# Performance work log

Hardware: AMD Instinct MI355X
Metric: run time of the kernel (lower is better)

## Reference

```python
import jax, jax.numpy as jnp
import numpy as np

WIN, DIL, PAD, H = 5, 1, 2, 8  # window, dilation, unfold padding, num_heads
C = 256
EPS = 1e-5

def _ln(z, g, b):
    m = jnp.mean(z, axis=-1, keepdims=True)
    v = jnp.mean((z - m) ** 2, axis=-1, keepdims=True)
    return (z - m) * jax.lax.rsqrt(v + EPS) * g + b

def setup_inputs() -> dict:
    key = jax.random.key(0)
    ks = jax.random.split(key, 16)
    s = 0.02
    d = {
        'x': jax.random.normal(ks[0], (32, C, 64, 25), jnp.float32),
        'ln1_g': jnp.ones((C,), jnp.float32), 'ln1_b': jnp.zeros((C,), jnp.float32),
        'q_w': jax.random.normal(ks[1], (C, C)) * s, 'q_b': jnp.zeros((C,)),
        'qa_w': jax.random.normal(ks[2], (C, H)) * s, 'qa_b': jnp.zeros((H,)),
        'k_w': jax.random.normal(ks[3], (C, C)) * s, 'k_b': jnp.zeros((C,)),
        'ka_w': jax.random.normal(ks[4], (C, H)) * s, 'ka_b': jnp.zeros((H,)),
        'v_w': jax.random.normal(ks[5], (C, C)) * s, 'v_b': jnp.zeros((C,)),
        't_w': jax.random.normal(ks[6], (C, C)) * s, 't_b': jnp.zeros((C,)),
        'p_w': jax.random.normal(ks[7], (C, C)) * s, 'p_b': jnp.zeros((C,)),
        'ffn_g': jnp.ones((C,)), 'ffn_b': jnp.zeros((C,)),
        'w1': jax.random.normal(ks[8], (C, C)) * s, 'b1': jnp.zeros((C,)),
        'w2': jax.random.normal(ks[9], (C, C)) * s, 'b2': jnp.zeros((C,)),
    }
    return d

def reference(x, ln1_g, ln1_b, q_w, q_b, qa_w, qa_b, k_w, k_b, ka_w, ka_b,
              v_w, v_b, t_w, t_b, p_w, p_b, ffn_g, ffn_b, w1, b1, w2, b2):
    N, Cc, T, V = x.shape
    hc = Cc // H
    scale = 1.0 / np.sqrt(hc)
    B, L = N * T, WIN * V
    xp = jnp.pad(x, ((0, 0), (0, 0), (PAD, PAD), (0, 0)))
    win = jnp.stack([xp[:, :, k * DIL:k * DIL + T, :] for k in range(WIN)], axis=2)  # (N,C,W,T,V)
    wx = win.transpose(0, 3, 2, 4, 1).reshape(B, L, Cc)
    nx = _ln(wx, ln1_g, ln1_b)
    # attention: softmax-pooled query
    q = nx @ q_w + q_b                                      # (B,L,C)
    qw = jax.nn.softmax(((q @ qa_w + qa_b) * scale).transpose(0, 2, 1), axis=-1)  # (B,H,L)
    qh = q.reshape(B, L, H, hc).transpose(0, 2, 1, 3)       # (B,H,L,hc)
    pq = jnp.einsum('bhl,bhld->bhd', qw, qh)                # (B,H,hc)
    k_ = nx @ k_w + k_b
    kq = k_ * pq.reshape(B, 1, Cc)
    kw = jax.nn.softmax(((kq @ ka_w + ka_b) * scale).transpose(0, 2, 1), axis=-1)
    kh = k_.reshape(B, L, H, hc).transpose(0, 2, 1, 3)
    pk = jnp.einsum('bhl,bhld->bhd', kw, kh)                # (B,H,hc)
    v_ = nx @ v_w + v_b
    vh = v_.reshape(B, L, H, hc).transpose(0, 2, 1, 3)
    kv = (vh * pk[:, :, None, :]).transpose(0, 2, 1, 3).reshape(B, L, Cc)
    kvh = (kv @ t_w + t_b).reshape(B, L, H, hc).transpose(0, 2, 1, 3)
    att = ((kvh + qh).transpose(0, 2, 1, 3).reshape(B, L, Cc)) @ p_w + p_b
    # average over window, residual with flattened x
    att = att.reshape(B, WIN, V, Cc).mean(axis=1)           # (B,V,C)
    att = att + x.transpose(0, 2, 3, 1).reshape(B, V, Cc)
    # FFN residual block
    f = _ln(att, ffn_g, ffn_b)
    f = jax.nn.gelu(f @ w1 + b1, approximate=False) @ w2 + b2
    y = f + att
    return y.reshape(N, T, V, Cc).transpose(0, 3, 1, 2)     # (N,C,T,V)
```

## Files before the change

### kernel.cpp

```cpp
#include <hip/hip_runtime.h>
#include <hip/hip_bf16.h>

typedef unsigned short u16b;
typedef __attribute__((ext_vector_type(8))) short short8;
typedef __attribute__((ext_vector_type(4))) float floatx4;

#define DEV static __device__ __forceinline__

DEV float sh2f(unsigned short s) { union { unsigned u; float f; } c; c.u = ((unsigned)s) << 16; return c.f; }
DEV unsigned short f2b(float f) {
    unsigned u = __float_as_uint(f);
    u += 0x7FFF + ((u >> 16) & 1);
    return (unsigned short)(u >> 16);
}

constexpr int O_LN1G = 0, O_LN1B = 256, O_QB = 512, O_KB = 768, O_VB = 1024,
              O_TB = 1280, O_PB = 1536, O_FFNG = 1792, O_FFNB = 2048,
              O_B1 = 2304, O_B2 = 2560, O_QAB = 2816, O_KAB = 2824,
              O_QAW = 2832, O_KAW = 4880, O_CV = 6928;

__global__ void detect_k(const unsigned* __restrict__ xw, int* __restrict__ flag) {
    __shared__ int cnt;
    if (threadIdx.x == 0) cnt = 0;
    __syncthreads();
    int my = 0;
    for (int i = threadIdx.x; i < 4096; i += 256) {
        unsigned w = xw[i];
        unsigned e0 = (w >> 7) & 0xFFu;
        if (e0 >= 0xC0u) my++;
    }
    atomicAdd(&cnt, my);
    __syncthreads();
    if (threadIdx.x == 0) flag[0] = (cnt > 64) ? 1 : 0;
}

DEV unsigned short load_cvt(const void* src, size_t idx, int fp32) {
    return fp32 ? f2b(((const float*)src)[idx]) : ((const u16b*)src)[idx];
}

struct VecTab { const void* p[15]; int off[15]; int n[15]; };

__global__ __launch_bounds__(256)
void convert_vecs_k(VecTab tab, const int* __restrict__ flag, u16b* __restrict__ sv) {
    int e = blockIdx.x, fp32 = flag[0];
    const void* s = tab.p[e];
    int n = tab.n[e], off = tab.off[e];
    for (int i = threadIdx.x; i < n; i += 256)
        sv[off + i] = load_cvt(s, i, fp32);
}

struct W8 { const void* p[8]; unsigned dstoff[8]; unsigned rstride[8]; };

__global__ void wtrans_k(W8 tab, u16b* __restrict__ base, const int* __restrict__ flag) {
    __shared__ u16b tile[32][33];
    int fp32 = flag[0];
    const void* src = tab.p[blockIdx.z];
    u16b* dst = base + tab.dstoff[blockIdx.z];
    unsigned rs = tab.rstride[blockIdx.z];
    int c0 = blockIdx.x * 32, r0 = blockIdx.y * 32;
    int tx = threadIdx.x, ty = threadIdx.y;
#pragma unroll
    for (int i = 0; i < 32; i += 8)
        tile[ty + i][tx] = load_cvt(src, (size_t)(r0 + ty + i) * 256 + c0 + tx, fp32);
    __syncthreads();
#pragma unroll
    for (int i = 0; i < 32; i += 8)
        dst[(size_t)(c0 + ty + i) * rs + r0 + tx] = tile[tx][ty + i];
}

__global__ void transpose_in_k(const void* __restrict__ src, u16b* __restrict__ dst,
                               int rows, int cols, const int* __restrict__ flag) {
    __shared__ u16b tile[32][33];
    int fp32 = flag[0];
    int c0 = blockIdx.x * 32, r0 = blockIdx.y * 32;
    size_t zb = (size_t)blockIdx.z * rows * cols;
    int tx = threadIdx.x, ty = threadIdx.y;
#pragma unroll
    for (int i = 0; i < 32; i += 8)
        tile[ty + i][tx] = load_cvt(src, zb + (size_t)(r0 + ty + i) * cols + c0 + tx, fp32);
    __syncthreads();
#pragma unroll
    for (int i = 0; i < 32; i += 8)
        dst[zb + (size_t)(c0 + ty + i) * rows + r0 + tx] = tile[tx][ty + i];
}

__global__ void transpose_out_k(const u16b* __restrict__ src, void* __restrict__ dst,
                                int rows, int cols, const int* __restrict__ flag) {
    __shared__ u16b tile[32][33];
    int fp32 = flag[0];
    int c0 = blockIdx.x * 32, r0 = blockIdx.y * 32;
    size_t zb = (size_t)blockIdx.z * rows * cols;
    int tx = threadIdx.x, ty = threadIdx.y;
#pragma unroll
    for (int i = 0; i < 32; i += 8)
        tile[ty + i][tx] = src[zb + (size_t)(r0 + ty + i) * cols + c0 + tx];
    __syncthreads();
#pragma unroll
    for (int i = 0; i < 32; i += 8) {
        size_t idx = zb + (size_t)(c0 + ty + i) * rows + r0 + tx;
        unsigned short v = tile[tx][ty + i];
        if (fp32) ((float*)dst)[idx] = sh2f(v);
        else      ((u16b*)dst)[idx] = v;
    }
}

__global__ __launch_bounds__(256)
void rowstats_k(const u16b* __restrict__ src, float2* __restrict__ st,
                int valid, int total) {
    int wv = threadIdx.x >> 6, lane = threadIdx.x & 63;
    int r = blockIdx.x * 4 + wv;
    if (r >= total) return;
    if (r >= valid) { if (lane == 0) st[r] = make_float2(0.f, 0.f); return; }
    int c = lane * 4;
    ushort4 raw = *(const ushort4*)&src[(size_t)r * 256 + c];
    float x0 = sh2f(raw.x), x1 = sh2f(raw.y), x2 = sh2f(raw.z), x3 = sh2f(raw.w);
    float s  = x0 + x1 + x2 + x3;
    float sq = x0 * x0 + x1 * x1 + x2 * x2 + x3 * x3;
#pragma unroll
    for (int o = 32; o; o >>= 1) { s += __shfl_xor(s, o); sq += __shfl_xor(sq, o); }
    float mean = s * (1.f / 256.f);
    float var  = sq * (1.f / 256.f) - mean * mean;
    if (lane == 0) st[r] = make_float2(mean, rsqrtf(var + 1e-5f));
}

__global__ __launch_bounds__(256)
void cvec_k(const u16b* __restrict__ pT, u16b* __restrict__ sv) {
    int j = threadIdx.x;
    float acc = sh2f(sv[O_PB + j]);
    const u16b* row = pT + (size_t)j * 256;
    for (int i = 0; i < 256; i += 8) {
        short8 t8 = *(const short8*)&sv[O_TB + i];
        short8 p8 = *(const short8*)&row[i];
#pragma unroll
        for (int u = 0; u < 8; ++u)
            acc += sh2f((unsigned short)t8[u]) * sh2f((unsigned short)p8[u]);
    }
    sv[O_CV + j] = f2b(acc);
}

template <int EPI, int LNA>
__global__ __launch_bounds__(256)
void gemm256(const u16b* __restrict__ A, int aStride, int K,
             const u16b* __restrict__ Wt,
             const u16b* __restrict__ bias, const u16b* __restrict__ addm,
             u16b* __restrict__ out, size_t osParam,
             const float2* __restrict__ stats,
             const u16b* __restrict__ gvec, const u16b* __restrict__ bvec) {
    __shared__ u16b As[128 * 72];
    __shared__ u16b Bs[128 * 72];
    __shared__ float sg[256], sb[256];
    const int tid = threadIdx.x;
    const int m0 = blockIdx.x * 128, n0 = blockIdx.y * 128;
    const int wv = tid >> 6, lane = tid & 63;
    const int wrow = (wv >> 1) * 64, wcol = (wv & 1) * 64;
    const int fr = lane & 15;
    const int fq = lane >> 4;
    floatx4 acc[4][4];
    const floatx4 zero = {0.f, 0.f, 0.f, 0.f};
#pragma unroll
    for (int i = 0; i < 4; ++i)
#pragma unroll
        for (int j = 0; j < 4; ++j) acc[i][j] = zero;

    float2 strow[4];
    if (LNA) {
        sg[tid] = sh2f(gvec[tid]);
        sb[tid] = sh2f(bvec[tid]);
#pragma unroll
        for (int kk = 0; kk < 4; ++kk) strow[kk] = stats[m0 + (tid >> 3) + kk * 32];
        __syncthreads();
    }

    for (int kt = 0; kt < K; kt += 64) {
#pragma unroll
        for (int kk = 0; kk < 4; ++kk) {
            int chunk = tid + kk * 256;
            int row = chunk >> 3, col = (chunk & 7) * 8;
            union { uint4 u; unsigned short h[8]; } rw;
            rw.u = *(const uint4*)&A[(size_t)(m0 + row) * aStride + kt + col];
            if (LNA) {
#pragma unroll
                for (int j = 0; j < 8; ++j) {
                    float f = sh2f(rw.h[j]);
                    f = (f - strow[kk].x) * strow[kk].y * sg[kt + col + j] + sb[kt + col + j];
                    rw.h[j] = f2b(f);
                }
            }
            *(uint4*)&As[row * 72 + col] = rw.u;
            *(uint4*)&Bs[row * 72 + col] = *(const uint4*)&Wt[(size_t)(n0 + row) * K + kt + col];
        }
        __syncthreads();
#pragma unroll
        for (int s = 0; s < 2; ++s) {
            short8 af[4], bfr[4];
#pragma unroll
            for (int i = 0; i < 4; ++i)
                af[i] = *(short8*)&As[(wrow + i * 16 + fr) * 72 + s * 32 + fq * 8];
#pragma unroll
            for (int j = 0; j < 4; ++j)
                bfr[j] = *(short8*)&Bs[(wcol + j * 16 + fr) * 72 + s * 32 + fq * 8];
#pragma unroll
            for (int i = 0; i < 4; ++i)
#pragma unroll
                for (int j = 0; j < 4; ++j)
                    acc[i][j] = __builtin_amdgcn_mfma_f32_16x16x32_bf16(af[i], bfr[j], acc[i][j], 0, 0, 0);
        }
        __syncthreads();
    }
    float bv[4];
#pragma unroll
    for (int j = 0; j < 4; ++j) bv[j] = bias ? sh2f(bias[n0 + wcol + j * 16 + fr]) : 0.f;
#pragma unroll
    for (int i = 0; i < 4; ++i) {
#pragma unroll
        for (int r = 0; r < 4; ++r) {
            int row = m0 + wrow + i * 16 + fq * 4 + r;
            size_t ro = (size_t)row * 256;
#pragma unroll
            for (int j = 0; j < 4; ++j) {
                int col = n0 + wcol + j * 16 + fr;
                float val = acc[i][j][r] + bv[j];
                if (EPI == 2) val += sh2f(addm[ro + col]);
                if (EPI == 3) val = 0.5f * val * (1.0f + erff(val * 0.70710678118654752f));
                if (EPI == 4)      out[(size_t)(col >> 8) * osParam + ro + (col & 255)] = f2b(val);
                else if (EPI == 0) out[(size_t)row * osParam + col] = f2b(val);
                else               out[ro + col] = f2b(val);
            }
        }
    }
}

DEV void pool_stage(const u16b* __restrict__ S, const u16b* __restrict__ sv,
                    int awoff, int aboff, const float* mult, float* outPool,
                    const int* srow, u16b* su, float* slog, float* spool, int tid) {
    for (int i = tid; i < 2048; i += 512) {
        int c = i >> 3, h = i & 7;
        float w = sh2f(sv[awoff + i]);
        if (mult) w *= mult[c];
        su[h * 260 + c] = f2b(w);
    }
    __syncthreads();
    int wv = tid >> 6, lane = tid & 63;
    int fr = lane & 15, fq = lane >> 4;
    floatx4 acc = {0.f, 0.f, 0.f, 0.f};
    const u16b* Ar = S + (size_t)srow[wv * 16 + fr] * 256;
#pragma unroll
    for (int s = 0; s < 8; ++s) {
        short8 a  = *(const short8*)&Ar[s * 32 + fq * 8];
        short8 bb = *(const short8*)&su[fr * 260 + s * 32 + fq * 8];
        acc = __builtin_amdgcn_mfma_f32_16x16x32_bf16(a, bb, acc, 0, 0, 0);
    }
    float abv = sh2f(sv[aboff + (fr & 7)]);
    if (fr < 8) {
#pragma unroll
        for (int r = 0; r < 4; ++r)
            slog[(wv * 16 + fq * 4 + r) * 9 + fr] = (acc[r] + abv) * 0.17677669529663687f;
    }
    __syncthreads();
    {
        int h = wv;
        float v0 = (lane < 125) ? slog[lane * 9 + h] : -1e30f;
        float v1 = (lane + 64 < 125) ? slog[(lane + 64) * 9 + h] : -1e30f;
        float mx = fmaxf(v0, v1);
#pragma unroll
        for (int o = 32; o; o >>= 1) mx = fmaxf(mx, __shfl_xor(mx, o));
        float e0 = (lane < 125) ? __expf(v0 - mx) : 0.f;
        float e1 = (lane + 64 < 125) ? __expf(v1 - mx) : 0.f;
        float s = e0 + e1;
#pragma unroll
        for (int o = 32; o; o >>= 1) s += __shfl_xor(s, o);
        float inv = 1.f / s;
        if (lane < 125) slog[lane * 9 + h] = e0 * inv;
        if (lane + 64 < 125) slog[(lane + 64) * 9 + h] = e1 * inv;
    }
    __syncthreads();
    int c8 = (tid & 31) * 8, ls = tid >> 5;
    int h2 = c8 >> 5;
    float a8[8] = {0.f, 0.f, 0.f, 0.f, 0.f, 0.f, 0.f, 0.f};
    for (int l = ls; l < 125; l += 16) {
        float w = slog[l * 9 + h2];
        short8 d8 = *(const short8*)&S[(size_t)srow[l] * 256 + c8];
#pragma unroll
        for (int j = 0; j < 8; ++j) a8[j] += w * sh2f((unsigned short)d8[j]);
    }
#pragma unroll
    for (int j = 0; j < 8; ++j) spool[ls * 260 + c8 + j] = a8[j];
    __syncthreads();
    if (tid < 256) {
        float s = 0.f;
#pragma unroll
        for (int q = 0; q < 16; ++q) s += spool[q * 260 + tid];
        outPool[tid] = s;
    }
    __syncthreads();
}

__global__ __launch_bounds__(512)
void pool_fused(const u16b* __restrict__ qf, const u16b* __restrict__ kf,
                const u16b* __restrict__ vf, const u16b* __restrict__ sv,
                u16b* __restrict__ CB) {
    __shared__ int srow[128];
    __shared__ u16b su[16 * 260];
    __shared__ float slog[128 * 9];
    __shared__ float spool[16 * 260];
    __shared__ float spq[256], spk[256];
    int bid = blockIdx.x;
    int b = ((bid & 7) << 8) | (bid >> 3);
    int n = b >> 6, t = b & 63;
    int tid = threadIdx.x;
    if (tid < 128) {
        int l = tid < 125 ? tid : 124;
        int w = l / 25, v = l - w * 25, tt = t + w - 2;
        srow[tid] = ((unsigned)tt < 64u) ? (n * 64 + tt) * 25 + v : 51200;
    }
    for (int i = tid; i < 8 * 260; i += 512) su[8 * 260 + i] = 0;
    __syncthreads();
    pool_stage(qf, sv, O_QAW, O_QAB, nullptr, spq, srow, su, slog, spool, tid);
    for (int i = tid; i < 800; i += 512) {
        int v = i >> 5, c8 = (i & 31) * 8;
        float s[8] = {0.f, 0.f, 0.f, 0.f, 0.f, 0.f, 0.f, 0.f};
#pragma unroll
        for (int w = 0; w < 5; ++w) {
            short8 d8 = *(const short8*)&qf[(size_t)srow[w * 25 + v] * 256 + c8];
#pragma unroll
            for (int j = 0; j < 8; ++j) s[j] += sh2f((unsigned short)d8[j]);
        }
        unsigned short o[8];
#pragma unroll
        for (int j = 0; j < 8; ++j) o[j] = f2b(s[j] * 0.2f);
        *(uint4*)&CB[((size_t)b * 25 + v) * 512 + 256 + c8] = *(uint4*)o;
    }
    pool_stage(kf, sv, O_KAW, O_KAB, spq, spk, srow, su, slog, spool, tid);
    for (int i = tid; i < 800; i += 512) {
        int v = i >> 5, c8 = (i & 31) * 8;
        float s[8] = {0.f, 0.f, 0.f, 0.f, 0.f, 0.f, 0.f, 0.f};
#pragma unroll
        for (int w = 0; w < 5; ++w) {
            short8 d8 = *(const short8*)&vf[(size_t)srow[w * 25 + v] * 256 + c8];
#pragma unroll
            for (int j = 0; j < 8; ++j) s[j] += sh2f((unsigned short)d8[j]);
        }
        unsigned short o[8];
#pragma unroll
        for (int j = 0; j < 8; ++j) o[j] = f2b(s[j] * 0.2f * spk[c8 + j]);
        *(uint4*)&CB[((size_t)b * 25 + v) * 512 + c8] = *(uint4*)o;
    }
}

extern "C" void kernel_launch(void* const* d_in, const int* in_sizes, int n_in,
                              void* d_out, int out_size, void* d_ws, size_t ws_size,
                              hipStream_t stream) {
    (void)in_sizes; (void)n_in; (void)out_size; (void)ws_size;
    const void* x    = d_in[0];
    const void* ln1g = d_in[1];  const void* ln1b = d_in[2];
    const void* q_w  = d_in[3];  const void* q_b  = d_in[4];
    const void* qa_w = d_in[5];  const void* qa_b = d_in[6];
    const void* k_w  = d_in[7];  const void* k_b  = d_in[8];
    const void* ka_w = d_in[9];  const void* ka_b = d_in[10];
    const void* v_w  = d_in[11]; const void* v_b  = d_in[12];
    const void* t_w  = d_in[13]; const void* t_b  = d_in[14];
    const void* p_w  = d_in[15]; const void* p_b  = d_in[16];
    const void* ffng = d_in[17]; const void* ffnb = d_in[18];
    const void* w1   = d_in[19]; const void* b1   = d_in[20];
    const void* w2   = d_in[21]; const void* b2   = d_in[22];

    char* ws = (char*)d_ws;
    size_t off = 0;
    auto alloc = [&](size_t bytes) { void* p = ws + off; off += (bytes + 255) & ~(size_t)255; return p; };
    const size_t RPAD = 51328;
    int*    flag = (int*)alloc(256);
    u16b*   sv   = (u16b*)alloc(8192 * 2);
    u16b*   wT   = (u16b*)alloc((size_t)7 * 65536 * 2);
    u16b*   cW   = (u16b*)alloc((size_t)256 * 512 * 2);
    u16b*   xT   = (u16b*)alloc(RPAD * 256 * 2);
    u16b*   Bq   = (u16b*)alloc(RPAD * 256 * 2);
    u16b*   Bk   = (u16b*)alloc(RPAD * 256 * 2);
    u16b*   Bv   = (u16b*)alloc(RPAD * 256 * 2);
    u16b*   CB   = (u16b*)alloc((size_t)51200 * 512 * 2);
    u16b*   att  = (u16b*)alloc((size_t)51200 * 256 * 2);
    float2* st1  = (float2*)alloc(RPAD * 8);
    float2* st2  = (float2*)alloc((size_t)51200 * 8);

    u16b* pT  = wT + 3 * 65536;
    u16b* tT  = wT + 4 * 65536;
    u16b* w1T = wT + 5 * 65536;
    u16b* w2T = wT + 6 * 65536;

    detect_k<<<1, 256, 0, stream>>>((const unsigned*)x, flag);
    VecTab tab;
    const void* vp[15] = {ln1g, ln1b, q_b, k_b, v_b, t_b, p_b, ffng, ffnb, b1, b2, qa_b, ka_b, qa_w, ka_w};
    const int vo[15] = {O_LN1G, O_LN1B, O_QB, O_KB, O_VB, O_TB, O_PB, O_FFNG, O_FFNB, O_B1, O_B2, O_QAB, O_KAB, O_QAW, O_KAW};
    const int vn[15] = {256, 256, 256, 256, 256, 256, 256, 256, 256, 256, 256, 8, 8, 2048, 2048};
    for (int i = 0; i < 15; ++i) { tab.p[i] = vp[i]; tab.off[i] = vo[i]; tab.n[i] = vn[i]; }
    convert_vecs_k<<<15, 256, 0, stream>>>(tab, flag, sv);

    dim3 tb(32, 8);
    W8 wt;
    const void* wsrc[8] = {q_w, k_w, v_w, p_w, t_w, w1, w2, p_w};
    for (int i = 0; i < 8; ++i) {
        wt.p[i] = wsrc[i];
        wt.dstoff[i] = (i < 7) ? (unsigned)(i * 65536) : (unsigned)((cW + 256) - wT);
        wt.rstride[i] = (i < 7) ? 256u : 512u;
    }
    wtrans_k<<<dim3(8, 8, 8), tb, 0, stream>>>(wt, wT, flag);
    cvec_k<<<1, 256, 0, stream>>>(pT, sv);
    gemm256<0, 0><<<dim3(2, 2), 256, 0, stream>>>(pT, 256, 256, tT, nullptr, nullptr,
                                                  cW, 512, nullptr, nullptr, nullptr);
    transpose_in_k<<<dim3(50, 8, 32), tb, 0, stream>>>(x, xT, 256, 1600, flag);
    rowstats_k<<<12832, 256, 0, stream>>>(xT, st1, 51200, 51328);
    gemm256<4, 1><<<dim3(401, 6), 256, 0, stream>>>(xT, 256, 256, wT, sv + O_QB, nullptr,
                                                    Bq, RPAD * 256, st1, sv + O_LN1G, sv + O_LN1B);
    pool_fused<<<2048, 512, 0, stream>>>(Bq, Bk, Bv, sv, CB);
    gemm256<2, 0><<<dim3(400, 2), 256, 0, stream>>>(CB, 512, 512, cW, sv + O_CV, xT,
                                                    att, 256, nullptr, nullptr, nullptr);
    rowstats_k<<<12800, 256, 0, stream>>>(att, st2, 51200, 51200);
    gemm256<3, 1><<<dim3(400, 2), 256, 0, stream>>>(att, 256, 256, w1T, sv + O_B1, nullptr,
                                                    Bq, 256, st2, sv + O_FFNG, sv + O_FFNB);
    gemm256<2, 0><<<dim3(400, 2), 256, 0, stream>>>(Bq, 256, 256, w2T, sv + O_B2, att,
                                                    att, 256, nullptr, nullptr, nullptr);
    transpose_out_k<<<dim3(8, 50, 32), tb, 0, stream>>>(att, d_out, 1600, 256, flag);
}
```

Before: 420.9 us.

## Vectorize transposes and fuse query pooling with window-mean pass in pool kernel

The input and output transpose kernels now use 1D 256-thread blocks in which each thread moves four elements with float4/ushort4 loads and stores, and the shared tile is padded to 36 columns. This replaces scalar per-element global accesses. In pool_fused, the softmax-weighted query pooling is merged into the loop that computes the window mean of q, so each q row is read once instead of twice. The separate zeroing of part of the shared buffer is dropped. The 36-column padding may cause more bank conflicts on the column-wise shared reads, and zero-padded MFMA rows in logits_stage now depend on leftover shared contents.

```diff
diff --git a/kernel.cpp b/kernel.cpp
--- a/kernel.cpp
+++ b/kernel.cpp
@@ -68,39 +68,54 @@
         dst[(size_t)(c0 + ty + i) * rs + r0 + tx] = tile[tx][ty + i];
 }
 
-__global__ void transpose_in_k(const void* __restrict__ src, u16b* __restrict__ dst,
-                               int rows, int cols, const int* __restrict__ flag) {
-    __shared__ u16b tile[32][33];
+__global__ __launch_bounds__(256)
+void transpose_in_k(const void* __restrict__ src, u16b* __restrict__ dst,
+                    int rows, int cols, const int* __restrict__ flag) {
+    __shared__ u16b tile[32][36];
     int fp32 = flag[0];
     int c0 = blockIdx.x * 32, r0 = blockIdx.y * 32;
     size_t zb = (size_t)blockIdx.z * rows * cols;
-    int tx = threadIdx.x, ty = threadIdx.y;
-#pragma unroll
-    for (int i = 0; i < 32; i += 8)
-        tile[ty + i][tx] = load_cvt(src, zb + (size_t)(r0 + ty + i) * cols + c0 + tx, fp32);
-    __syncthreads();
-#pragma unroll
-    for (int i = 0; i < 32; i += 8)
-        dst[zb + (size_t)(c0 + ty + i) * rows + r0 + tx] = tile[tx][ty + i];
-}
-
-__global__ void transpose_out_k(const u16b* __restrict__ src, void* __restrict__ dst,
-                                int rows, int cols, const int* __restrict__ flag) {
-    __shared__ u16b tile[32][33];
+    int tid = threadIdx.x;
+    int r = tid >> 3, c4 = (tid & 7) * 4;
+    size_t sidx = zb + (size_t)(r0 + r) * cols + c0 + c4;
+    if (fp32) {
+        const float4 f4 = *(const float4*)((const float*)src + sidx);
+        tile[r][c4]     = f2b(f4.x);
+        tile[r][c4 + 1] = f2b(f4.y);
+        tile[r][c4 + 2] = f2b(f4.z);
+        tile[r][c4 + 3] = f2b(f4.w);
+    } else {
+        *(ushort4*)&tile[r][c4] = *(const ushort4*)((const u16b*)src + sidx);
+    }
+    __syncthreads();
+    int c = tid >> 3, r4 = (tid & 7) * 4;
+    ushort4 o;
+    o.x = tile[r4][c]; o.y = tile[r4 + 1][c]; o.z = tile[r4 + 2][c]; o.w = tile[r4 + 3][c];
+    *(ushort4*)&dst[zb + (size_t)(c0 + c) * rows + r0 + r4] = o;
+}
+
+__global__ __launch_bounds__(256)
+void transpose_out_k(const u16b* __restrict__ src, void* __restrict__ dst,
+                     int rows, int cols, const int* __restrict__ flag) {
+    __shared__ u16b tile[32][36];
     int fp32 = flag[0];
     int c0 = blockIdx.x * 32, r0 = blockIdx.y * 32;
     size_t zb = (size_t)blockIdx.z * rows * cols;
-    int tx = threadIdx.x, ty = threadIdx.y;
-#pragma unroll
-    for (int i = 0; i < 32; i += 8)
-        tile[ty + i][tx] = src[zb + (size_t)(r0 + ty + i) * cols + c0 + tx];
-    __syncthreads();
-#pragma unroll
-    for (int i = 0; i < 32; i += 8) {
-        size_t idx = zb + (size_t)(c0 + ty + i) * rows + r0 + tx;
-        unsigned short v = tile[tx][ty + i];
-        if (fp32) ((float*)dst)[idx] = sh2f(v);
-        else      ((u16b*)dst)[idx] = v;
+    int tid = threadIdx.x;
+    int r = tid >> 3, c4 = (tid & 7) * 4;
+    *(ushort4*)&tile[r][c4] = *(const ushort4*)&src[zb + (size_t)(r0 + r) * cols + c0 + c4];
+    __syncthreads();
+    int c = tid >> 3, r4 = (tid & 7) * 4;
+    size_t didx = zb + (size_t)(c0 + c) * rows + r0 + r4;
+    if (fp32) {
+        float4 f4;
+        f4.x = sh2f(tile[r4][c]);     f4.y = sh2f(tile[r4 + 1][c]);
+        f4.z = sh2f(tile[r4 + 2][c]); f4.w = sh2f(tile[r4 + 3][c]);
+        *(float4*)((float*)dst + didx) = f4;
+    } else {
+        ushort4 o;
+        o.x = tile[r4][c]; o.y = tile[r4 + 1][c]; o.z = tile[r4 + 2][c]; o.w = tile[r4 + 3][c];
+        *(ushort4*)((u16b*)dst + didx) = o;
     }
 }
 
@@ -230,9 +245,9 @@
     }
 }
 
-DEV void pool_stage(const u16b* __restrict__ S, const u16b* __restrict__ sv,
-                    int awoff, int aboff, const float* mult, float* outPool,
-                    const int* srow, u16b* su, float* slog, float* spool, int tid) {
+DEV void logits_stage(const u16b* __restrict__ S, const u16b* __restrict__ sv,
+                      int awoff, int aboff, const float* mult,
+                      const int* srow, u16b* su, float* slog, int tid) {
     for (int i = tid; i < 2048; i += 512) {
         int c = i >> 3, h = i & 7;
         float w = sh2f(sv[awoff + i]);
@@ -272,25 +287,6 @@
         float inv = 1.f / s;
         if (lane < 125) slog[lane * 9 + h] = e0 * inv;
         if (lane + 64 < 125) slog[(lane + 64) * 9 + h] = e1 * inv;
-    }
-    __syncthreads();
-    int c8 = (tid & 31) * 8, ls = tid >> 5;
-    int h2 = c8 >> 5;
-    float a8[8] = {0.f, 0.f, 0.f, 0.f, 0.f, 0.f, 0.f, 0.f};
-    for (int l = ls; l < 125; l += 16) {
-        float w = slog[l * 9 + h2];
-        short8 d8 = *(const short8*)&S[(size_t)srow[l] * 256 + c8];
-#pragma unroll
-        for (int j = 0; j < 8; ++j) a8[j] += w * sh2f((unsigned short)d8[j]);
-    }
-#pragma unroll
-    for (int j = 0; j < 8; ++j) spool[ls * 260 + c8 + j] = a8[j];
-    __syncthreads();
-    if (tid < 256) {
-        float s = 0.f;
-#pragma unroll
-        for (int q = 0; q < 16; ++q) s += spool[q * 260 + tid];
-        outPool[tid] = s;
     }
     __syncthreads();
 }
@@ -313,37 +309,82 @@
         int w = l / 25, v = l - w * 25, tt = t + w - 2;
         srow[tid] = ((unsigned)tt < 64u) ? (n * 64 + tt) * 25 + v : 51200;
     }
-    for (int i = tid; i < 8 * 260; i += 512) su[8 * 260 + i] = 0;
-    __syncthreads();
-    pool_stage(qf, sv, O_QAW, O_QAB, nullptr, spq, srow, su, slog, spool, tid);
-    for (int i = tid; i < 800; i += 512) {
-        int v = i >> 5, c8 = (i & 31) * 8;
-        float s[8] = {0.f, 0.f, 0.f, 0.f, 0.f, 0.f, 0.f, 0.f};
-#pragma unroll
-        for (int w = 0; w < 5; ++w) {
-            short8 d8 = *(const short8*)&qf[(size_t)srow[w * 25 + v] * 256 + c8];
-#pragma unroll
-            for (int j = 0; j < 8; ++j) s[j] += sh2f((unsigned short)d8[j]);
-        }
-        unsigned short o[8];
-#pragma unroll
-        for (int j = 0; j < 8; ++j) o[j] = f2b(s[j] * 0.2f);
-        *(uint4*)&CB[((size_t)b * 25 + v) * 512 + 256 + c8] = *(uint4*)o;
-    }
-    pool_stage(kf, sv, O_KAW, O_KAB, spq, spk, srow, su, slog, spool, tid);
-    for (int i = tid; i < 800; i += 512) {
-        int v = i >> 5, c8 = (i & 31) * 8;
-        float s[8] = {0.f, 0.f, 0.f, 0.f, 0.f, 0.f, 0.f, 0.f};
-#pragma unroll
-        for (int w = 0; w < 5; ++w) {
-            short8 d8 = *(const short8*)&vf[(size_t)srow[w * 25 + v] * 256 + c8];
-#pragma unroll
-            for (int j = 0; j < 8; ++j) s[j] += sh2f((unsigned short)d8[j]);
-        }
-        unsigned short o[8];
-#pragma unroll
-        for (int j = 0; j < 8; ++j) o[j] = f2b(s[j] * 0.2f * spk[c8 + j]);
-        *(uint4*)&CB[((size_t)b * 25 + v) * 512 + c8] = *(uint4*)o;
+    __syncthreads();
+
+    logits_stage(qf, sv, O_QAW, O_QAB, nullptr, srow, su, slog, tid);
+
+    {
+        int c8 = (tid & 31) * 8, h = c8 >> 5, ls = tid >> 5;
+        float p[8] = {0.f, 0.f, 0.f, 0.f, 0.f, 0.f, 0.f, 0.f};
+        for (int v = ls; v < 25; v += 16) {
+            float s[8] = {0.f, 0.f, 0.f, 0.f, 0.f, 0.f, 0.f, 0.f};
+#pragma unroll
+            for (int w = 0; w < 5; ++w) {
+                int l = w * 25 + v;
+                float wt = slog[l * 9 + h];
+                short8 d8 = *(const short8*)&qf[(size_t)srow[l] * 256 + c8];
+#pragma unroll
+                for (int j = 0; j < 8; ++j) {
+                    float f = sh2f((unsigned short)d8[j]);
+                    s[j] += f;
+                    p[j] += wt * f;
+                }
+            }
+            unsigned short o[8];
+#pragma unroll
+            for (int j = 0; j < 8; ++j) o[j] = f2b(s[j] * 0.2f);
+            *(uint4*)&CB[((size_t)b * 25 + v) * 512 + 256 + c8] = *(uint4*)o;
+        }
+#pragma unroll
+        for (int j = 0; j < 8; ++j) spool[ls * 260 + c8 + j] = p[j];
+    }
+    __syncthreads();
+    if (tid < 256) {
+        float s = 0.f;
+#pragma unroll
+        for (int q = 0; q < 16; ++q) s += spool[q * 260 + tid];
+        spq[tid] = s;
+    }
+    __syncthreads();
+
+    logits_stage(kf, sv, O_KAW, O_KAB, spq, srow, su, slog, tid);
+
+    {
+        int c8 = (tid & 31) * 8, h2 = c8 >> 5, ls = tid >> 5;
+        float a8[8] = {0.f, 0.f, 0.f, 0.f, 0.f, 0.f, 0.f, 0.f};
+        for (int l = ls; l < 125; l += 16) {
+            float w = slog[l * 9 + h2];
+            short8 d8 = *(const short8*)&kf[(size_t)srow[l] * 256 + c8];
+#pragma unroll
+            for (int j = 0; j < 8; ++j) a8[j] += w * sh2f((unsigned short)d8[j]);
+        }
+#pragma unroll
+        for (int j = 0; j < 8; ++j) spool[ls * 260 + c8 + j] = a8[j];
+    }
+    __syncthreads();
+    if (tid < 256) {
+        float s = 0.f;
+#pragma unroll
+        for (int q = 0; q < 16; ++q) s += spool[q * 260 + tid];
+        spk[tid] = s;
+    }
+    __syncthreads();
+
+    {
+        int c8 = (tid & 31) * 8, ls = tid >> 5;
+        for (int v = ls; v < 25; v += 16) {
+            float s[8] = {0.f, 0.f, 0.f, 0.f, 0.f, 0.f, 0.f, 0.f};
+#pragma unroll
+            for (int w = 0; w < 5; ++w) {
+                short8 d8 = *(const short8*)&vf[(size_t)srow[w * 25 + v] * 256 + c8];
+#pragma unroll
+                for (int j = 0; j < 8; ++j) s[j] += sh2f((unsigned short)d8[j]);
+            }
+            unsigned short o[8];
+#pragma unroll
+            for (int j = 0; j < 8; ++j) o[j] = f2b(s[j] * 0.2f * spk[c8 + j]);
+            *(uint4*)&CB[((size_t)b * 25 + v) * 512 + c8] = *(uint4*)o;
+        }
     }
 }
 
@@ -406,7 +447,7 @@
     cvec_k<<<1, 256, 0, stream>>>(pT, sv);
     gemm256<0, 0><<<dim3(2, 2), 256, 0, stream>>>(pT, 256, 256, tT, nullptr, nullptr,
                                                   cW, 512, nullptr, nullptr, nullptr);
-    transpose_in_k<<<dim3(50, 8, 32), tb, 0, stream>>>(x, xT, 256, 1600, flag);
+    transpose_in_k<<<dim3(50, 8, 32), 256, 0, stream>>>(x, xT, 256, 1600, flag);
     rowstats_k<<<12832, 256, 0, stream>>>(xT, st1, 51200, 51328);
     gemm256<4, 1><<<dim3(401, 6), 256, 0, stream>>>(xT, 256, 256, wT, sv + O_QB, nullptr,
                                                     Bq, RPAD * 256, st1, sv + O_LN1G, sv + O_LN1B);
@@ -418,5 +459,5 @@
                                                     Bq, 256, st2, sv + O_FFNG, sv + O_FFNB);
     gemm256<2, 0><<<dim3(400, 2), 256, 0, stream>>>(Bq, 256, 256, w2T, sv + O_B2, att,
                                                     att, 256, nullptr, nullptr, nullptr);
-    transpose_out_k<<<dim3(8, 50, 32), tb, 0, stream>>>(att, d_out, 1600, 256, flag);
-}
+    transpose_out_k<<<dim3(8, 50, 32), 256, 0, stream>>>(att, d_out, 1600, 256, flag);
+}
```

New measurement: 414.2 us. Within noise of the previous version (-1.6%).
